# Optimization experiments

Measured on AMD Instinct MI355X. Metric: run time of the kernel, lower is better.

Reference implementation:

```python
import jax, jax.numpy as jnp
import numpy as np

B, S, H, L, D, DI = 4, 32, 8, 128, 512, 2048
EPS = 1e-6
TEMP = float(D) ** 0.5


def layer_norm(x, g, b):
    mu = jnp.mean(x, axis=-1, keepdims=True)
    var = jnp.mean((x - mu) ** 2, axis=-1, keepdims=True)
    return (x - mu) * jax.lax.rsqrt(var + EPS) * g + b


def setup_inputs() -> dict:
    key = jax.random.key(0)
    ks = jax.random.split(key, 8)
    x = jax.random.normal(ks[0], (B, S, L, D), jnp.float32)
    mask = jax.random.randint(ks[1], (B, S, L), 0, 2, jnp.int32)
    # learned params
    w = jax.random.normal(ks[2], (1, 1, H, L, D), jnp.float32) * (1.0 / np.sqrt(D))
    v_w = jax.random.normal(ks[3], (D, D), jnp.float32) * 0.02   # nn.Linear weight (out,in)
    ln_g = jnp.ones((D,), jnp.float32)
    ln_b = jnp.zeros((D,), jnp.float32)
    w1 = jax.random.normal(ks[4], (DI, D), jnp.float32) * 0.02
    b1 = jnp.zeros((DI,), jnp.float32)
    w2 = jax.random.normal(ks[5], (D, DI), jnp.float32) * 0.02
    b2 = jnp.zeros((D,), jnp.float32)
    fln_g = jnp.ones((D,), jnp.float32)
    fln_b = jnp.zeros((D,), jnp.float32)
    return {"x": x, "mask": mask, "w": w, "v_w": v_w, "ln_g": ln_g, "ln_b": ln_b,
            "w1": w1, "b1": b1, "w2": w2, "b2": b2, "fln_g": fln_g, "fln_b": fln_b}


def reference(x, mask, w, v_w, ln_g, ln_b, w1, b1, w2, b2, fln_g, fln_b):
    # attn logits: broadcast mul + reduce over d_model == einsum over d
    attn = jnp.einsum('bsld,hld->bshl', x, w[0, 0]) / TEMP           # (B,S,H,L)
    attn = jnp.where(mask[:, :, None, :] == 0, -1e9, attn)
    attn = jax.nn.softmax(attn, axis=-1)                              # dropout: eval mode
    v = jnp.einsum('bsld,ed->bsle', x, v_w)                           # Linear no bias: x @ W.T
    out = jnp.einsum('bsld,bshl->bshd', v, attn)                      # weighted sum readout
    out = layer_norm(out, ln_g, ln_b)
    # PositionwiseFeedForward with residual + LayerNorm
    h = jax.nn.relu(jnp.einsum('bshd,fd->bshf', out, w1) + b1)
    y = jnp.einsum('bshf,df->bshd', h, w2) + b2 + out
    y = layer_norm(y, fln_g, fln_b)
    return y, attn
```

## Files before the change

### kernel.cpp

```cpp
#include <hip/hip_runtime.h>
#include <hip/hip_bf16.h>

#define BB 4
#define SS 32
#define HH 8
#define LL 128
#define DD 512
#define DI 2048
#define EPSN 1e-6f
#define INV_TEMP 0.04419417382415922f

#define NLOGW_BLK 512
#define NCAST_GRAN ((DI*DD/4)*2 + (DD*DD/4))
#define NCAST_BLK (NCAST_GRAN / 256)

#define NROW (BB*SS*HH)
#define SLICE ((size_t)NROW * DD)
#define NAVL_BLK 64

typedef __attribute__((ext_vector_type(8))) short short8;
typedef __attribute__((ext_vector_type(4))) float float4v;

static __device__ __forceinline__ unsigned short f2b(float f) {
  __hip_bfloat16 h = __float2bfloat16(f);
  return *(unsigned short*)&h;
}

static __device__ __forceinline__ size_t pk(int m, int k, int K) {
  return ((((size_t)(m >> 4) * (K >> 5) + (k >> 5)) * 4 + ((k >> 3) & 3)) * 16
          + (m & 15)) * 8 + (k & 7);
}

__global__ __launch_bounds__(256) void pre_kernel(
    const float* __restrict__ x, const int* __restrict__ mask,
    const float* __restrict__ w, const float* __restrict__ w1,
    const float* __restrict__ w2, const float* __restrict__ v_w,
    unsigned short* __restrict__ w1b, unsigned short* __restrict__ w2b,
    unsigned short* __restrict__ v_wb, float* __restrict__ logits) {
  int blk = blockIdx.x;
  if (blk < NLOGW_BLK) {
    int wv = threadIdx.x >> 6, lane = threadIdx.x & 63;
    int p   = blk * 4 + wv;
    int l   = p >> 4;
    int bsg = p & 15;

    float4 wr[HH][2];
#pragma unroll
    for (int h = 0; h < HH; ++h) {
      const float4* wp = (const float4*)(w + ((size_t)h * LL + l) * DD) + lane * 2;
      wr[h][0] = wp[0];
      wr[h][1] = wp[1];
    }

#pragma unroll 2
    for (int i = 0; i < 8; ++i) {
      int bs = bsg * 8 + i;
      const float4* xr = (const float4*)(x + ((size_t)bs * LL + l) * DD) + lane * 2;
      float4 x0 = xr[0], x1 = xr[1];
      float acc[HH];
#pragma unroll
      for (int h = 0; h < HH; ++h) {
        acc[h] = x0.x * wr[h][0].x + x0.y * wr[h][0].y +
                 x0.z * wr[h][0].z + x0.w * wr[h][0].w +
                 x1.x * wr[h][1].x + x1.y * wr[h][1].y +
                 x1.z * wr[h][1].z + x1.w * wr[h][1].w;
      }
#pragma unroll
      for (int off = 32; off > 0; off >>= 1) {
#pragma unroll
        for (int h = 0; h < HH; ++h) acc[h] += __shfl_xor(acc[h], off);
      }
      if (lane == 0) {
        int msk = mask[bs * LL + l];
#pragma unroll
        for (int h = 0; h < HH; ++h) {
          float lg = msk ? acc[h] * INV_TEMP : -1e9f;
          logits[((size_t)bs * HH + h) * LL + l] = lg;
        }
      }
    }
  } else {
    const int n1 = (DI * DD) / 4;
    const int n2 = n1;
    int i = (blk - NLOGW_BLK) * 256 + threadIdx.x;
    float4 v;
    unsigned short* dst;
    size_t base;
    if (i < n1) {
      v = ((const float4*)w1)[i];
      dst = w1b;
      base = pk(i >> 7, (i & 127) * 4, DD);
    } else if (i < n1 + n2) {
      int j = i - n1;
      v = ((const float4*)w2)[j];
      dst = w2b;
      base = pk(j >> 9, (j & 511) * 4, DI);
    } else {
      int j = i - n1 - n2;
      v = ((const float4*)v_w)[j];
      dst = v_wb;
      base = pk(j >> 7, (j & 127) * 4, DD);
    }
    dst[base + 0] = f2b(v.x);
    dst[base + 1] = f2b(v.y);
    dst[base + 2] = f2b(v.z);
    dst[base + 3] = f2b(v.w);
  }
}

__global__ __launch_bounds__(512) void attn_v_ln_kernel(
    const float* __restrict__ x, const float* __restrict__ logits,
    const unsigned short* __restrict__ v_wb, const float* __restrict__ ln_g,
    const float* __restrict__ ln_b, float* __restrict__ attn_out,
    float* __restrict__ o_ln, unsigned short* __restrict__ o_lnb) {
  int blk = blockIdx.x;
  int t = threadIdx.x, wv = t >> 6, lane = t & 63;
  int bs0 = blk * 2;

  __shared__ __align__(16) float sattnT[LL][20];
  __shared__ __align__(16) unsigned short apk[16 * DD];
  __shared__ float wstat[8][16][2];
  __shared__ float rstat[16][2];

#pragma unroll
  for (int rr = 0; rr < 2; ++rr) {
    int r = wv * 2 + rr;
    int bs = bs0 + (r >> 3), h = r & 7;
    const float* lg = logits + ((size_t)bs * HH + h) * LL;
    float v0 = lg[lane], v1 = lg[lane + 64];
    float m = fmaxf(v0, v1);
#pragma unroll
    for (int off = 32; off > 0; off >>= 1) m = fmaxf(m, __shfl_xor(m, off));
    float e0 = __expf(v0 - m), e1 = __expf(v1 - m);
    float s = e0 + e1;
#pragma unroll
    for (int off = 32; off > 0; off >>= 1) s += __shfl_xor(s, off);
    float inv = 1.f / s;
    e0 *= inv; e1 *= inv;
    sattnT[lane][r]      = e0;
    sattnT[lane + 64][r] = e1;
    float* ao = attn_out + ((size_t)bs * HH + h) * LL;
    ao[lane]      = e0;
    ao[lane + 64] = e1;
  }
  __syncthreads();

  {
    int ecl  = t & 127;
    int half = (t >> 7) & 1;
    int hg   = t >> 8;
    int bs   = bs0 + half;
    const float4* xb4 = (const float4*)(x + (size_t)bs * LL * DD) + ecl;
    float acc[4][4];
#pragma unroll
    for (int h = 0; h < 4; ++h)
#pragma unroll
      for (int j = 0; j < 4; ++j) acc[h][j] = 0.f;
#pragma unroll 4
    for (int l = 0; l < LL; ++l) {
      float4 xv = xb4[l * (DD / 4)];
      float4 a0 = *(const float4*)&sattnT[l][half * 8 + hg * 4];
      acc[0][0] += a0.x * xv.x; acc[0][1] += a0.x * xv.y;
      acc[0][2] += a0.x * xv.z; acc[0][3] += a0.x * xv.w;
      acc[1][0] += a0.y * xv.x; acc[1][1] += a0.y * xv.y;
      acc[1][2] += a0.y * xv.z; acc[1][3] += a0.y * xv.w;
      acc[2][0] += a0.z * xv.x; acc[2][1] += a0.z * xv.y;
      acc[2][2] += a0.z * xv.z; acc[2][3] += a0.z * xv.w;
      acc[3][0] += a0.w * xv.x; acc[3][1] += a0.w * xv.y;
      acc[3][2] += a0.w * xv.z; acc[3][3] += a0.w * xv.w;
    }
    int e0i = ecl * 4;
    unsigned pbase = ((e0i >> 5) * 4 + ((e0i >> 3) & 3)) * 128 + (e0i & 7);
#pragma unroll
    for (int h = 0; h < 4; ++h) {
      int m = half * 8 + hg * 4 + h;
#pragma unroll
      for (int j = 0; j < 4; ++j) apk[pbase + m * 8 + j] = f2b(acc[h][j]);
    }
  }
  __syncthreads();

  int lm = lane & 15, lq = lane >> 4;
  int n0 = wv * 64;
  const short8* A8 = (const short8*)apk;
  const short8* B8 = (const short8*)v_wb;
  float4v acc3[4];
#pragma unroll
  for (int nf = 0; nf < 4; ++nf) acc3[nf] = (float4v){0.f, 0.f, 0.f, 0.f};
#pragma unroll 4
  for (int c = 0; c < 16; ++c) {
    short8 a = A8[c * 64 + lane];
#pragma unroll
    for (int nf = 0; nf < 4; ++nf) {
      short8 b = B8[((size_t)((n0 >> 4) + nf) * 16 + c) * 64 + lane];
      acc3[nf] = __builtin_amdgcn_mfma_f32_16x16x32_bf16(a, b, acc3[nf], 0, 0, 0);
    }
  }

  float srow[4], qrow[4];
#pragma unroll
  for (int r = 0; r < 4; ++r) {
    float s = 0.f, q = 0.f;
#pragma unroll
    for (int nf = 0; nf < 4; ++nf) { float v = acc3[nf][r]; s += v; q += v * v; }
#pragma unroll
    for (int off = 1; off < 16; off <<= 1) {
      s += __shfl_xor(s, off);
      q += __shfl_xor(q, off);
    }
    srow[r] = s; qrow[r] = q;
  }
  if (lm == 0) {
#pragma unroll
    for (int r = 0; r < 4; ++r) {
      wstat[wv][lq * 4 + r][0] = srow[r];
      wstat[wv][lq * 4 + r][1] = qrow[r];
    }
  }
  __syncthreads();
  if (t < 16) {
    float S = 0.f, Q = 0.f;
#pragma unroll
    for (int w8 = 0; w8 < 8; ++w8) { S += wstat[w8][t][0]; Q += wstat[w8][t][1]; }
    float mu  = S * (1.f / DD);
    float var = Q * (1.f / DD) - mu * mu;
    rstat[t][0] = mu;
    rstat[t][1] = rsqrtf(var + EPSN);
  }
  __syncthreads();
#pragma unroll
  for (int nf = 0; nf < 4; ++nf) {
    int col = n0 + nf * 16 + lm;
    float g = ln_g[col], bcol = ln_b[col];
#pragma unroll
    for (int r = 0; r < 4; ++r) {
      int row = lq * 4 + r;
      float v = (acc3[nf][r] - rstat[row][0]) * rstat[row][1] * g + bcol;
      int grow = blk * 16 + row;
      o_ln[(size_t)grow * DD + col] = v;
      o_lnb[pk(grow, col, DD)] = f2b(v);
    }
  }
}

__global__ __launch_bounds__(256) void gemm1_kernel(
    const unsigned short* __restrict__ o_lnb, const unsigned short* __restrict__ w1b,
    const float* __restrict__ b1, unsigned short* __restrict__ h1b) {
  int blk = blockIdx.x;
  int nt = blk & 31, mt = blk >> 5;
  int wv = threadIdx.x >> 6, lane = threadIdx.x & 63;
  int lm = lane & 15, lq = lane >> 4;

  int m0 = mt * 64 + wv * 16;
  int n0 = nt * 64;
  const short8* A8 = (const short8*)o_lnb + (size_t)(m0 >> 4) * 16 * 64;
  const short8* B8 = (const short8*)w1b;

  float4v acc[4];
#pragma unroll
  for (int nf = 0; nf < 4; ++nf) acc[nf] = (float4v){0.f, 0.f, 0.f, 0.f};

#pragma unroll 4
  for (int c = 0; c < 16; ++c) {
    short8 a = A8[(size_t)c * 64 + lane];
#pragma unroll
    for (int nf = 0; nf < 4; ++nf) {
      short8 b = B8[((size_t)((n0 >> 4) + nf) * 16 + c) * 64 + lane];
      acc[nf] = __builtin_amdgcn_mfma_f32_16x16x32_bf16(a, b, acc[nf], 0, 0, 0);
    }
  }

#pragma unroll
  for (int nf = 0; nf < 4; ++nf) {
    int col = n0 + nf * 16 + lm;
    float bb = b1[col];
#pragma unroll
    for (int r = 0; r < 4; ++r) {
      int row = m0 + lq * 4 + r;
      h1b[pk(row, col, DI)] = f2b(fmaxf(acc[nf][r] + bb, 0.f));
    }
  }
}

__global__ __launch_bounds__(256) void gemm2_kernel(
    const unsigned short* __restrict__ h1b, const unsigned short* __restrict__ w2b,
    float* __restrict__ ypart) {
  int blk = blockIdx.x;
  int nt = blk & 7, mt = (blk >> 3) & 15, kslice = blk >> 7;
  int wv = threadIdx.x >> 6, lane = threadIdx.x & 63;
  int lm = lane & 15, lq = lane >> 4;

  int m0 = mt * 64 + wv * 16;
  int n0 = nt * 64;
  const short8* A8 = (const short8*)h1b + (size_t)(m0 >> 4) * 64 * 64;
  const short8* B8 = (const short8*)w2b;

  float4v acc[4];
#pragma unroll
  for (int nf = 0; nf < 4; ++nf) acc[nf] = (float4v){0.f, 0.f, 0.f, 0.f};

#pragma unroll 4
  for (int ci = 0; ci < 16; ++ci) {
    int c = kslice * 16 + ci;
    short8 a = A8[(size_t)c * 64 + lane];
#pragma unroll
    for (int nf = 0; nf < 4; ++nf) {
      short8 b = B8[((size_t)((n0 >> 4) + nf) * 64 + c) * 64 + lane];
      acc[nf] = __builtin_amdgcn_mfma_f32_16x16x32_bf16(a, b, acc[nf], 0, 0, 0);
    }
  }

  float* outp = ypart + (size_t)kslice * SLICE;
#pragma unroll
  for (int nf = 0; nf < 4; ++nf) {
    int col = n0 + nf * 16 + lm;
#pragma unroll
    for (int r = 0; r < 4; ++r)
      outp[(size_t)(m0 + lq * 4 + r) * DD + col] = acc[nf][r];
  }
}

__global__ __launch_bounds__(256) void ln_final_kernel(
    const float* __restrict__ ypart, const float* __restrict__ o_ln,
    const float* __restrict__ b2, const float* __restrict__ fln_g,
    const float* __restrict__ fln_b, float* __restrict__ y_out) {
  int wv = threadIdx.x >> 6, lane = threadIdx.x & 63;
  int row = blockIdx.x * 4 + wv;

  const float* p0 = ypart + (size_t)row * DD;
  const float* ol = o_ln + (size_t)row * DD;
  float vals[8];
  float sum = 0.f, sq = 0.f;
#pragma unroll
  for (int k = 0; k < 8; ++k) {
    int d = lane + 64 * k;
    float v = p0[d] + p0[SLICE + d] + p0[2 * SLICE + d] + p0[3 * SLICE + d] +
              b2[d] + ol[d];
    vals[k] = v;
    sum += v;
    sq += v * v;
  }
#pragma unroll
  for (int off = 32; off > 0; off >>= 1) {
    sum += __shfl_xor(sum, off);
    sq  += __shfl_xor(sq, off);
  }
  float mu  = sum * (1.f / DD);
  float var = sq * (1.f / DD) - mu * mu;
  float rs  = rsqrtf(var + EPSN);
  float* yo = y_out + (size_t)row * DD;
#pragma unroll
  for (int k = 0; k < 8; ++k) {
    int d = lane + 64 * k;
    yo[d] = (vals[k] - mu) * rs * fln_g[d] + fln_b[d];
  }
}

extern "C" void kernel_launch(void* const* d_in, const int* in_sizes, int n_in,
                              void* d_out, int out_size, void* d_ws, size_t ws_size,
                              hipStream_t stream) {
  const float* x     = (const float*)d_in[0];
  const int*   mask  = (const int*)d_in[1];
  const float* w     = (const float*)d_in[2];
  const float* v_w   = (const float*)d_in[3];
  const float* ln_g  = (const float*)d_in[4];
  const float* ln_b  = (const float*)d_in[5];
  const float* w1    = (const float*)d_in[6];
  const float* b1    = (const float*)d_in[7];
  const float* w2    = (const float*)d_in[8];
  const float* b2    = (const float*)d_in[9];
  const float* fln_g = (const float*)d_in[10];
  const float* fln_b = (const float*)d_in[11];

  float* y    = (float*)d_out;
  float* attn = y + (size_t)BB * SS * HH * DD;

  char* ws = (char*)d_ws;
  float*          o_ln   = (float*)(ws);
  unsigned short* o_lnb  = (unsigned short*)(ws + 2097152);
  unsigned short* w1b    = (unsigned short*)(ws + 3145728);
  unsigned short* w2b    = (unsigned short*)(ws + 5242880);
  unsigned short* h1b    = (unsigned short*)(ws + 7340032);
  float*          ypart  = (float*)(ws + 11534336);
  unsigned short* v_wb   = (unsigned short*)(ws + 19922944);
  float*          logits = (float*)(ws + 29884416);

  pre_kernel<<<NLOGW_BLK + NCAST_BLK, 256, 0, stream>>>(
      x, mask, w, w1, w2, v_w, w1b, w2b, v_wb, logits);
  attn_v_ln_kernel<<<NAVL_BLK, 512, 0, stream>>>(
      x, logits, v_wb, ln_g, ln_b, attn, o_ln, o_lnb);
  gemm1_kernel<<<512, 256, 0, stream>>>(o_lnb, w1b, b1, h1b);
  gemm2_kernel<<<512, 256, 0, stream>>>(h1b, w2b, ypart);
  ln_final_kernel<<<256, 256, 0, stream>>>(ypart, o_ln, b2, fln_g, fln_b, y);
}
```

Measured before the change: 159.3 us.

## Process one (b,s) per attention block to double grid parallelism

The fused softmax/attn-weighted-sum/V-projection/LayerNorm kernel now handles a single (b,s) pair (8 head rows) per block instead of two, doubling the block count to 128. Each thread computes one d-column for all 8 heads with scalar x loads instead of a 4x4 register tile, and the MFMA A tile pads the unused 8 rows with zeros. The aim is to spread this kernel across more compute units. In exchange, half the MFMA work is wasted on zero rows, v_wb is re-read by twice as many blocks, and the x loads are narrower.

```diff
diff --git a/kernel.cpp b/kernel.cpp
--- a/kernel.cpp
+++ b/kernel.cpp
@@ -16,7 +16,7 @@
 
 #define NROW (BB*SS*HH)
 #define SLICE ((size_t)NROW * DD)
-#define NAVL_BLK 64
+#define NAVL_BLK 128
 
 typedef __attribute__((ext_vector_type(8))) short short8;
 typedef __attribute__((ext_vector_type(4))) float float4v;
@@ -113,19 +113,16 @@
     const unsigned short* __restrict__ v_wb, const float* __restrict__ ln_g,
     const float* __restrict__ ln_b, float* __restrict__ attn_out,
     float* __restrict__ o_ln, unsigned short* __restrict__ o_lnb) {
-  int blk = blockIdx.x;
+  int bs = blockIdx.x;
   int t = threadIdx.x, wv = t >> 6, lane = t & 63;
-  int bs0 = blk * 2;
 
   __shared__ __align__(16) float sattnT[LL][20];
   __shared__ __align__(16) unsigned short apk[16 * DD];
-  __shared__ float wstat[8][16][2];
-  __shared__ float rstat[16][2];
-
-#pragma unroll
-  for (int rr = 0; rr < 2; ++rr) {
-    int r = wv * 2 + rr;
-    int bs = bs0 + (r >> 3), h = r & 7;
+  __shared__ float wstat[8][8][2];
+  __shared__ float rstat[8][2];
+
+  {
+    int h = wv;
     const float* lg = logits + ((size_t)bs * HH + h) * LL;
     float v0 = lg[lane], v1 = lg[lane + 64];
     float m = fmaxf(v0, v1);
@@ -137,8 +134,8 @@
     for (int off = 32; off > 0; off >>= 1) s += __shfl_xor(s, off);
     float inv = 1.f / s;
     e0 *= inv; e1 *= inv;
-    sattnT[lane][r]      = e0;
-    sattnT[lane + 64][r] = e1;
+    sattnT[lane][h]      = e0;
+    sattnT[lane + 64][h] = e1;
     float* ao = attn_out + ((size_t)bs * HH + h) * LL;
     ao[lane]      = e0;
     ao[lane + 64] = e1;
@@ -146,37 +143,26 @@
   __syncthreads();
 
   {
-    int ecl  = t & 127;
-    int half = (t >> 7) & 1;
-    int hg   = t >> 8;
-    int bs   = bs0 + half;
-    const float4* xb4 = (const float4*)(x + (size_t)bs * LL * DD) + ecl;
-    float acc[4][4];
-#pragma unroll
-    for (int h = 0; h < 4; ++h)
-#pragma unroll
-      for (int j = 0; j < 4; ++j) acc[h][j] = 0.f;
+    int e = t;
+    const float* xb = x + (size_t)bs * LL * DD + e;
+    float acc[8];
+#pragma unroll
+    for (int h = 0; h < 8; ++h) acc[h] = 0.f;
 #pragma unroll 4
     for (int l = 0; l < LL; ++l) {
-      float4 xv = xb4[l * (DD / 4)];
-      float4 a0 = *(const float4*)&sattnT[l][half * 8 + hg * 4];
-      acc[0][0] += a0.x * xv.x; acc[0][1] += a0.x * xv.y;
-      acc[0][2] += a0.x * xv.z; acc[0][3] += a0.x * xv.w;
-      acc[1][0] += a0.y * xv.x; acc[1][1] += a0.y * xv.y;
-      acc[1][2] += a0.y * xv.z; acc[1][3] += a0.y * xv.w;
-      acc[2][0] += a0.z * xv.x; acc[2][1] += a0.z * xv.y;
-      acc[2][2] += a0.z * xv.z; acc[2][3] += a0.z * xv.w;
-      acc[3][0] += a0.w * xv.x; acc[3][1] += a0.w * xv.y;
-      acc[3][2] += a0.w * xv.z; acc[3][3] += a0.w * xv.w;
-    }
-    int e0i = ecl * 4;
-    unsigned pbase = ((e0i >> 5) * 4 + ((e0i >> 3) & 3)) * 128 + (e0i & 7);
-#pragma unroll
-    for (int h = 0; h < 4; ++h) {
-      int m = half * 8 + hg * 4 + h;
-#pragma unroll
-      for (int j = 0; j < 4; ++j) apk[pbase + m * 8 + j] = f2b(acc[h][j]);
-    }
+      float xv = xb[(size_t)l * DD];
+      float4 a0 = *(const float4*)&sattnT[l][0];
+      float4 a1 = *(const float4*)&sattnT[l][4];
+      acc[0] += a0.x * xv; acc[1] += a0.y * xv;
+      acc[2] += a0.z * xv; acc[3] += a0.w * xv;
+      acc[4] += a1.x * xv; acc[5] += a1.y * xv;
+      acc[6] += a1.z * xv; acc[7] += a1.w * xv;
+    }
+    unsigned base = ((e >> 5) * 4 + ((e >> 3) & 3)) * 128 + (e & 7);
+#pragma unroll
+    for (int h = 0; h < 8; ++h) apk[base + h * 8] = f2b(acc[h]);
+#pragma unroll
+    for (int h = 8; h < 16; ++h) apk[base + h * 8] = 0;
   }
   __syncthreads();
 
@@ -210,7 +196,7 @@
     }
     srow[r] = s; qrow[r] = q;
   }
-  if (lm == 0) {
+  if (lm == 0 && lq < 2) {
 #pragma unroll
     for (int r = 0; r < 4; ++r) {
       wstat[wv][lq * 4 + r][0] = srow[r];
@@ -218,7 +204,7 @@
     }
   }
   __syncthreads();
-  if (t < 16) {
+  if (t < 8) {
     float S = 0.f, Q = 0.f;
 #pragma unroll
     for (int w8 = 0; w8 < 8; ++w8) { S += wstat[w8][t][0]; Q += wstat[w8][t][1]; }
@@ -228,17 +214,19 @@
     rstat[t][1] = rsqrtf(var + EPSN);
   }
   __syncthreads();
-#pragma unroll
-  for (int nf = 0; nf < 4; ++nf) {
-    int col = n0 + nf * 16 + lm;
-    float g = ln_g[col], bcol = ln_b[col];
-#pragma unroll
-    for (int r = 0; r < 4; ++r) {
-      int row = lq * 4 + r;
-      float v = (acc3[nf][r] - rstat[row][0]) * rstat[row][1] * g + bcol;
-      int grow = blk * 16 + row;
-      o_ln[(size_t)grow * DD + col] = v;
-      o_lnb[pk(grow, col, DD)] = f2b(v);
+  if (lq < 2) {
+#pragma unroll
+    for (int nf = 0; nf < 4; ++nf) {
+      int col = n0 + nf * 16 + lm;
+      float g = ln_g[col], bcol = ln_b[col];
+#pragma unroll
+      for (int r = 0; r < 4; ++r) {
+        int row = lq * 4 + r;
+        float v = (acc3[nf][r] - rstat[row][0]) * rstat[row][1] * g + bcol;
+        int grow = bs * 8 + row;
+        o_ln[(size_t)grow * DD + col] = v;
+        o_lnb[pk(grow, col, DD)] = f2b(v);
+      }
     }
   }
 }
```

After: 155.7 us. 2.3% less time.
